# Kernel optimization log

Hardware: AMD Instinct MI355X
Metric: run time of the kernel (lower is better)

The kernel has to match this reference:

```python
import jax, jax.numpy as jnp
import numpy as np

LOG2 = float(np.log(2.0))
NEG_INF = float('-inf')


def log1mexp(x):
    # numerically accurate log(1 - exp(x)) for x < 0
    return jnp.where(x > -LOG2, jnp.log(-jnp.expm1(x)), jnp.log1p(-jnp.exp(x)))


def encode_input_log(pos):
    neg = log1mexp(pos)
    # interleave [pos_i, neg_i] then prepend constants [-inf (log 0), 0 (log 1)]
    result = jnp.stack([pos, neg], axis=1).reshape(-1)
    constants = jnp.array([NEG_INF, 0.0], dtype=pos.dtype)
    return jnp.concatenate([constants, result])


def sum_layer(x, ptrs, csr, n):
    # product node in log semiring: segment-sum of gathered log-values
    return jax.ops.segment_sum(x[ptrs], csr, num_segments=n)


def logsum_layer(x, ptrs, csr, n, epsilon=1e-15):
    # sum node in log semiring: numerically stable segment log-sum-exp
    g = x[ptrs]
    m = jax.lax.stop_gradient(jax.ops.segment_max(g, csr, num_segments=n))
    z = g - m[csr]
    z = jnp.nan_to_num(z, nan=0.0, posinf=jnp.inf, neginf=-jnp.inf)  # (-inf)-(-inf) -> 0
    s = jax.ops.segment_sum(jnp.exp(z), csr, num_segments=n) + epsilon
    return jnp.log(s) + m


def setup_inputs() -> dict:
    key = jax.random.key(0)
    n_vars = 2_000_000
    deg = 4
    Ns = [4_000_000, 2_000_000, 1_000_000, 500_000]
    sizes_in = [2 + 2 * n_vars] + Ns[:-1]
    ks = jax.random.split(key, 1 + len(Ns))
    # log-probabilities strictly in (log eps, log(1-eps)) so log1mexp is finite
    u = jax.random.uniform(ks[0], (n_vars,), dtype=jnp.float32, minval=1e-6, maxval=1.0 - 1e-6)
    inp = {"weights": jnp.log(u)}
    for i, n in enumerate(Ns):
        e = n * deg
        inp[f"ptrs{i}"] = jax.random.randint(ks[i + 1], (e,), 0, sizes_in[i], dtype=jnp.int32)
        inp[f"csr{i}"] = jnp.repeat(jnp.arange(n, dtype=jnp.int32), deg)  # unrolled CSR, fan-in=deg
        inp[f"n{i}"] = n
    return inp


def reference(weights, ptrs0, csr0, ptrs1, csr1, ptrs2, csr2, ptrs3, csr3, n0, n1, n2, n3):
    x = encode_input_log(weights)
    x = sum_layer(x, ptrs0, csr0, n0)      # layer 0: product (even)
    x = logsum_layer(x, ptrs1, csr1, n1)   # layer 1: sum (odd)
    x = sum_layer(x, ptrs2, csr2, n2)      # layer 2: product
    x = logsum_layer(x, ptrs3, csr3, n3)   # layer 3: sum
    return x
```

## Files before the change

kernel.cpp:

```cpp
#include <hip/hip_runtime.h>
#include <math.h>

#define NEG_INF (-INFINITY)

typedef int      v4i __attribute__((ext_vector_type(4)));
typedef float    v4f __attribute__((ext_vector_type(4)));
typedef _Float16 v4h __attribute__((ext_vector_type(4)));

__device__ __forceinline__ float fast_log1mexp(float v) {
    if (v > -0.125f) {
        float e = v * (1.0f + v * (0.5f + v * (0.16666667f + v * 0.041666667f)));
        return __logf(-e);
    }
    return __logf(1.0f - __expf(v));
}

__global__ __launch_bounds__(256) void cvt_kernel(const float* __restrict__ w,
                                                  _Float16* __restrict__ wh, int n) {
    int i = blockIdx.x * blockDim.x + threadIdx.x;
    int n4 = n >> 2;
    if (i < n4) {
        v4f v = reinterpret_cast<const v4f*>(w)[i];
        v4h o;
        o.x = (_Float16)v.x; o.y = (_Float16)v.y;
        o.z = (_Float16)v.z; o.w = (_Float16)v.w;
        reinterpret_cast<v4h*>(wh)[i] = o;
    }
    int base = n4 << 2;
    if (i < (n - base)) wh[base + i] = (_Float16)w[base + i];
}

__device__ __forceinline__ int widx(int p) { int j = (p >> 1) - 1; return j < 0 ? 0 : j; }
__device__ __forceinline__ float fixw(int p, float v) {
    float r = (p & 1) ? fast_log1mexp(v) : v;
    if (p < 2) r = (p == 0) ? NEG_INF : 0.0f;
    return r;
}

__global__ __launch_bounds__(256) void sum4_enc_kernel(const _Float16* __restrict__ wh,
                                                       const v4i* __restrict__ ptrs,
                                                       _Float16* __restrict__ y, int n, int h) {
    int t = blockIdx.x * blockDim.x + threadIdx.x;
    if (t >= h) return;
    int i0 = t, i1 = t + h, i2 = t + 2 * h, i3 = t + 3 * h;
    int c1 = i1 < n ? i1 : 0, c2 = i2 < n ? i2 : 0, c3 = i3 < n ? i3 : 0;
    v4i p0 = __builtin_nontemporal_load(ptrs + i0);
    v4i p1 = __builtin_nontemporal_load(ptrs + c1);
    v4i p2 = __builtin_nontemporal_load(ptrs + c2);
    v4i p3 = __builtin_nontemporal_load(ptrs + c3);
    float g00 = (float)wh[widx(p0.x)], g01 = (float)wh[widx(p0.y)];
    float g02 = (float)wh[widx(p0.z)], g03 = (float)wh[widx(p0.w)];
    float g10 = (float)wh[widx(p1.x)], g11 = (float)wh[widx(p1.y)];
    float g12 = (float)wh[widx(p1.z)], g13 = (float)wh[widx(p1.w)];
    float g20 = (float)wh[widx(p2.x)], g21 = (float)wh[widx(p2.y)];
    float g22 = (float)wh[widx(p2.z)], g23 = (float)wh[widx(p2.w)];
    float g30 = (float)wh[widx(p3.x)], g31 = (float)wh[widx(p3.y)];
    float g32 = (float)wh[widx(p3.z)], g33 = (float)wh[widx(p3.w)];
    float s0 = (fixw(p0.x, g00) + fixw(p0.y, g01)) + (fixw(p0.z, g02) + fixw(p0.w, g03));
    float s1 = (fixw(p1.x, g10) + fixw(p1.y, g11)) + (fixw(p1.z, g12) + fixw(p1.w, g13));
    float s2 = (fixw(p2.x, g20) + fixw(p2.y, g21)) + (fixw(p2.z, g22) + fixw(p2.w, g23));
    float s3 = (fixw(p3.x, g30) + fixw(p3.y, g31)) + (fixw(p3.z, g32) + fixw(p3.w, g33));
    __builtin_nontemporal_store((_Float16)s0, y + i0);
    if (i1 < n) __builtin_nontemporal_store((_Float16)s1, y + i1);
    if (i2 < n) __builtin_nontemporal_store((_Float16)s2, y + i2);
    if (i3 < n) __builtin_nontemporal_store((_Float16)s3, y + i3);
}

__device__ __forceinline__ float lse4(float a, float b, float c, float d) {
    float m = fmaxf(fmaxf(a, b), fmaxf(c, d));
    if (m == NEG_INF) return NEG_INF;
    float s = __expf(a - m) + __expf(b - m) + __expf(c - m) + __expf(d - m) + 1e-15f;
    return __logf(s) + m;
}

__global__ __launch_bounds__(256) void logsum4_l1_kernel(const _Float16* __restrict__ x,
                                                         const v4i* __restrict__ ptrs,
                                                         _Float16* __restrict__ y,
                                                         int n, int h) {
    int t = blockIdx.x * blockDim.x + threadIdx.x;
    if (t >= h) return;
    int i0 = t, i1 = t + h;
    int c1 = i1 < n ? i1 : 0;
    v4i p0 = __builtin_nontemporal_load(ptrs + i0);
    v4i p1 = __builtin_nontemporal_load(ptrs + c1);
    float a0 = (float)x[p0.x], b0 = (float)x[p0.y];
    float e0 = (float)x[p0.z], d0 = (float)x[p0.w];
    float a1 = (float)x[p1.x], b1 = (float)x[p1.y];
    float e1 = (float)x[p1.z], d1 = (float)x[p1.w];
    float s0 = lse4(a0, b0, e0, d0);
    float s1 = lse4(a1, b1, e1, d1);
    __builtin_nontemporal_store((_Float16)s0, y + i0);
    if (i1 < n) __builtin_nontemporal_store((_Float16)s1, y + i1);
}

__global__ __launch_bounds__(256) void sum4_h2h_kernel(const _Float16* __restrict__ x,
                                                       const v4i* __restrict__ ptrs,
                                                       _Float16* __restrict__ y, int n, int h) {
    int t = blockIdx.x * blockDim.x + threadIdx.x;
    if (t >= h) return;
    int i0 = t, i1 = t + h;
    int c1 = i1 < n ? i1 : 0;
    v4i p0 = __builtin_nontemporal_load(ptrs + i0);
    v4i p1 = __builtin_nontemporal_load(ptrs + c1);
    float s0 = ((float)x[p0.x] + (float)x[p0.y]) + ((float)x[p0.z] + (float)x[p0.w]);
    float s1 = ((float)x[p1.x] + (float)x[p1.y]) + ((float)x[p1.z] + (float)x[p1.w]);
    __builtin_nontemporal_store((_Float16)s0, y + i0);
    if (i1 < n) __builtin_nontemporal_store((_Float16)s1, y + i1);
}

__global__ __launch_bounds__(256) void logsum4_h2f_kernel(const _Float16* __restrict__ x,
                                                          const v4i* __restrict__ ptrs,
                                                          float* __restrict__ y, int n) {
    int t = blockIdx.x * blockDim.x + threadIdx.x;
    if (t >= n) return;
    v4i p = __builtin_nontemporal_load(ptrs + t);
    float r = lse4((float)x[p.x], (float)x[p.y], (float)x[p.z], (float)x[p.w]);
    __builtin_nontemporal_store(r, y + t);
}

extern "C" void kernel_launch(void* const* d_in, const int* in_sizes, int n_in,
                              void* d_out, int out_size, void* d_ws, size_t ws_size,
                              hipStream_t stream) {
    const float* w     = (const float*)d_in[0];
    const v4i*   ptrs0 = (const v4i*)d_in[1];
    const v4i*   ptrs1 = (const v4i*)d_in[4];
    const v4i*   ptrs2 = (const v4i*)d_in[7];
    const v4i*   ptrs3 = (const v4i*)d_in[10];

    const int n_vars = in_sizes[0];
    const int n0 = in_sizes[1] / 4;
    const int n1 = in_sizes[4] / 4;
    const int n2 = in_sizes[7] / 4;
    const int n3 = in_sizes[10] / 4;

    char* ws = (char*)d_ws;
    size_t off = 0;
    _Float16* wh = (_Float16*)(ws + off); off += ((size_t)n_vars * 2 + 255) & ~(size_t)255;
    _Float16* y0 = (_Float16*)(ws + off); off += ((size_t)n0 * 2 + 255) & ~(size_t)255;
    _Float16* y1 = (_Float16*)(ws + off); off += ((size_t)n1 * 2 + 255) & ~(size_t)255;
    _Float16* y2 = (_Float16*)(ws + off);
    float* out = (float*)d_out;

    const int B = 256;
    int hc = (n_vars + 3) / 4;
    int h0 = (n0 + 3) / 4;
    int h1 = (n1 + 1) / 2;
    int h2 = (n2 + 1) / 2;

    cvt_kernel        <<<(hc + B - 1) / B, B, 0, stream>>>(w, wh, n_vars);
    sum4_enc_kernel   <<<(h0 + B - 1) / B, B, 0, stream>>>(wh, ptrs0, y0, n0, h0);
    logsum4_l1_kernel <<<(h1 + B - 1) / B, B, 0, stream>>>(y0, ptrs1, y1, n1, h1);
    sum4_h2h_kernel   <<<(h2 + B - 1) / B, B, 0, stream>>>(y1, ptrs2, y2, n2, h2);
    logsum4_h2f_kernel<<<(n3 + B - 1) / B, B, 0, stream>>>(y2, ptrs3, out, n3);
}
```

Baseline: 371.1 us.

## Split layer-1 gathers into low/high index halves and merge partial log-sum-exps

The layer-0 product kernel is launched twice, once per half of its output range, using a new offset argument. The layer-1 log-sum kernel now handles four nodes per thread in two passes: first only children in the lower half of the input, then, after a block barrier, only those in the upper half. The two partial log-sum-exps are merged at the end. The aim is to keep each pass's gather working set (about half of the 8 MB fp16 buffer) resident in cache. In exchange it doubles the number of gather and exp instructions, since out-of-range children are clamped and masked to -inf. The block barrier also cannot keep other blocks in phase, so the locality gain may be small.

```diff
diff --git a/kernel.cpp b/kernel.cpp
--- a/kernel.cpp
+++ b/kernel.cpp
@@ -39,10 +39,11 @@
 
 __global__ __launch_bounds__(256) void sum4_enc_kernel(const _Float16* __restrict__ wh,
                                                        const v4i* __restrict__ ptrs,
-                                                       _Float16* __restrict__ y, int n, int h) {
+                                                       _Float16* __restrict__ y,
+                                                       int off, int n, int h) {
     int t = blockIdx.x * blockDim.x + threadIdx.x;
     if (t >= h) return;
-    int i0 = t, i1 = t + h, i2 = t + 2 * h, i3 = t + 3 * h;
+    int i0 = off + t, i1 = i0 + h, i2 = i0 + 2 * h, i3 = i0 + 3 * h;
     int c1 = i1 < n ? i1 : 0, c2 = i2 < n ? i2 : 0, c3 = i3 < n ? i3 : 0;
     v4i p0 = __builtin_nontemporal_load(ptrs + i0);
     v4i p1 = __builtin_nontemporal_load(ptrs + c1);
@@ -66,31 +67,71 @@
     if (i3 < n) __builtin_nontemporal_store((_Float16)s3, y + i3);
 }
 
-__device__ __forceinline__ float lse4(float a, float b, float c, float d) {
+__device__ __forceinline__ float plse4(float a, float b, float c, float d) {
     float m = fmaxf(fmaxf(a, b), fmaxf(c, d));
     if (m == NEG_INF) return NEG_INF;
-    float s = __expf(a - m) + __expf(b - m) + __expf(c - m) + __expf(d - m) + 1e-15f;
+    float s = __expf(a - m) + __expf(b - m) + __expf(c - m) + __expf(d - m);
     return __logf(s) + m;
 }
 
-__global__ __launch_bounds__(256) void logsum4_l1_kernel(const _Float16* __restrict__ x,
-                                                         const v4i* __restrict__ ptrs,
-                                                         _Float16* __restrict__ y,
-                                                         int n, int h) {
-    int t = blockIdx.x * blockDim.x + threadIdx.x;
-    if (t >= h) return;
-    int i0 = t, i1 = t + h;
-    int c1 = i1 < n ? i1 : 0;
+__device__ __forceinline__ float merge_lse(float LA, float LB) {
+    float m = fmaxf(LA, LB);
+    if (m == NEG_INF) return NEG_INF;
+    float s = __expf(LA - m) + __expf(LB - m) + 1e-15f;
+    return __logf(s) + m;
+}
+
+__device__ __forceinline__ float gsel_lo(const _Float16* __restrict__ x, int p, int half) {
+    int q = p < half ? p : 0;
+    float v = (float)x[q];
+    return p < half ? v : NEG_INF;
+}
+__device__ __forceinline__ float gsel_hi(const _Float16* __restrict__ x, int p, int half) {
+    int q = p >= half ? p : half;
+    float v = (float)x[q];
+    return p >= half ? v : NEG_INF;
+}
+
+__global__ __launch_bounds__(256) void l1_fused_kernel(const _Float16* __restrict__ x,
+                                                       const v4i* __restrict__ ptrs,
+                                                       _Float16* __restrict__ y,
+                                                       int n, int h, int half) {
+    int t = blockIdx.x * blockDim.x + threadIdx.x;
+    bool act = t < h;
+    int tt = act ? t : 0;
+    int i0 = tt, i1 = tt + h, i2 = tt + 2 * h, i3 = tt + 3 * h;
+    int c1 = i1 < n ? i1 : 0, c2 = i2 < n ? i2 : 0, c3 = i3 < n ? i3 : 0;
     v4i p0 = __builtin_nontemporal_load(ptrs + i0);
     v4i p1 = __builtin_nontemporal_load(ptrs + c1);
-    float a0 = (float)x[p0.x], b0 = (float)x[p0.y];
-    float e0 = (float)x[p0.z], d0 = (float)x[p0.w];
-    float a1 = (float)x[p1.x], b1 = (float)x[p1.y];
-    float e1 = (float)x[p1.z], d1 = (float)x[p1.w];
-    float s0 = lse4(a0, b0, e0, d0);
-    float s1 = lse4(a1, b1, e1, d1);
-    __builtin_nontemporal_store((_Float16)s0, y + i0);
-    if (i1 < n) __builtin_nontemporal_store((_Float16)s1, y + i1);
+    v4i p2 = __builtin_nontemporal_load(ptrs + c2);
+    v4i p3 = __builtin_nontemporal_load(ptrs + c3);
+
+    float la0 = plse4(gsel_lo(x, p0.x, half), gsel_lo(x, p0.y, half),
+                      gsel_lo(x, p0.z, half), gsel_lo(x, p0.w, half));
+    float la1 = plse4(gsel_lo(x, p1.x, half), gsel_lo(x, p1.y, half),
+                      gsel_lo(x, p1.z, half), gsel_lo(x, p1.w, half));
+    float la2 = plse4(gsel_lo(x, p2.x, half), gsel_lo(x, p2.y, half),
+                      gsel_lo(x, p2.z, half), gsel_lo(x, p2.w, half));
+    float la3 = plse4(gsel_lo(x, p3.x, half), gsel_lo(x, p3.y, half),
+                      gsel_lo(x, p3.z, half), gsel_lo(x, p3.w, half));
+
+    __syncthreads();
+
+    float s0 = merge_lse(la0, plse4(gsel_hi(x, p0.x, half), gsel_hi(x, p0.y, half),
+                                    gsel_hi(x, p0.z, half), gsel_hi(x, p0.w, half)));
+    float s1 = merge_lse(la1, plse4(gsel_hi(x, p1.x, half), gsel_hi(x, p1.y, half),
+                                    gsel_hi(x, p1.z, half), gsel_hi(x, p1.w, half)));
+    float s2 = merge_lse(la2, plse4(gsel_hi(x, p2.x, half), gsel_hi(x, p2.y, half),
+                                    gsel_hi(x, p2.z, half), gsel_hi(x, p2.w, half)));
+    float s3 = merge_lse(la3, plse4(gsel_hi(x, p3.x, half), gsel_hi(x, p3.y, half),
+                                    gsel_hi(x, p3.z, half), gsel_hi(x, p3.w, half)));
+
+    if (act) {
+        __builtin_nontemporal_store((_Float16)s0, y + i0);
+        if (i1 < n) __builtin_nontemporal_store((_Float16)s1, y + i1);
+        if (i2 < n) __builtin_nontemporal_store((_Float16)s2, y + i2);
+        if (i3 < n) __builtin_nontemporal_store((_Float16)s3, y + i3);
+    }
 }
 
 __global__ __launch_bounds__(256) void sum4_h2h_kernel(const _Float16* __restrict__ x,
@@ -108,6 +149,13 @@
     if (i1 < n) __builtin_nontemporal_store((_Float16)s1, y + i1);
 }
 
+__device__ __forceinline__ float lse4(float a, float b, float c, float d) {
+    float m = fmaxf(fmaxf(a, b), fmaxf(c, d));
+    if (m == NEG_INF) return NEG_INF;
+    float s = __expf(a - m) + __expf(b - m) + __expf(c - m) + __expf(d - m) + 1e-15f;
+    return __logf(s) + m;
+}
+
 __global__ __launch_bounds__(256) void logsum4_h2f_kernel(const _Float16* __restrict__ x,
                                                           const v4i* __restrict__ ptrs,
                                                           float* __restrict__ y, int n) {
@@ -143,13 +191,17 @@
 
     const int B = 256;
     int hc = (n_vars + 3) / 4;
-    int h0 = (n0 + 3) / 4;
-    int h1 = (n1 + 1) / 2;
+    int mid0 = n0 / 2;
+    int hA = (mid0 + 3) / 4;
+    int hB = (n0 - mid0 + 3) / 4;
+    int h1 = (n1 + 3) / 4;
     int h2 = (n2 + 1) / 2;
+    int half0 = n0 / 2;
 
     cvt_kernel        <<<(hc + B - 1) / B, B, 0, stream>>>(w, wh, n_vars);
-    sum4_enc_kernel   <<<(h0 + B - 1) / B, B, 0, stream>>>(wh, ptrs0, y0, n0, h0);
-    logsum4_l1_kernel <<<(h1 + B - 1) / B, B, 0, stream>>>(y0, ptrs1, y1, n1, h1);
+    sum4_enc_kernel   <<<(hA + B - 1) / B, B, 0, stream>>>(wh, ptrs0, y0, 0, mid0, hA);
+    sum4_enc_kernel   <<<(hB + B - 1) / B, B, 0, stream>>>(wh, ptrs0, y0, mid0, n0, hB);
+    l1_fused_kernel   <<<(h1 + B - 1) / B, B, 0, stream>>>(y0, ptrs1, y1, n1, h1, half0);
     sum4_h2h_kernel   <<<(h2 + B - 1) / B, B, 0, stream>>>(y1, ptrs2, y2, n2, h2);
     logsum4_h2f_kernel<<<(n3 + B - 1) / B, B, 0, stream>>>(y2, ptrs3, out, n3);
 }
```

Measured after the change: 367.9 us. Within noise of the previous version (-0.9%).
